# Optimization experiments

Hardware: AMD Instinct MI355X
Metric: run time of the kernel (lower is better)

Reference implementation:

```python
import jax, jax.numpy as jnp
import numpy as np

N = 50000          # neuron_count
NNZ = 1_600_000    # edges (avg degree 32)
B = 32             # batch
L = 3              # CONNECTOME_LAYER_NUMBER


def setup_inputs() -> dict:
    key = jax.random.key(0)
    k1, k2, k3, k4, k5 = jax.random.split(key, 5)
    x = jax.random.normal(k1, (B, N), dtype=jnp.float32)
    adj_vals = jax.random.uniform(k2, (NNZ,), dtype=jnp.float32)
    w_vals = jax.random.uniform(k3, (NNZ,), dtype=jnp.float32)
    bias = jnp.ones((N,), dtype=jnp.float32)
    row = jax.random.randint(k4, (NNZ,), 0, N, dtype=jnp.int32)
    col = jax.random.randint(k5, (NNZ,), 0, N, dtype=jnp.int32)
    return {"x": x, "adj_vals": adj_vals, "w_vals": w_vals, "bias": bias,
            "row": row, "col": col}


def _spmm(vals, row, col, dense, n):
    # (sparse NxN) @ dense [N, B] via gather + segment_sum scatter
    contrib = vals[:, None] * dense[col]          # [nnz, B]
    return jax.ops.segment_sum(contrib, row, num_segments=n)


def reference(x, adj_vals, w_vals, bias, row, col):
    # Original per layer: x = ((A @ W) @ x^T)^T + bias.
    # We use associativity: (A @ W) @ x^T == A @ (W @ x^T), avoiding the
    # explicit SpGEMM while computing the same linear map.
    n = bias.shape[0]
    xt = x.T                                      # [N, B]
    for _ in range(L):
        wx = _spmm(w_vals, row, col, xt, n)       # W @ x^T -> [N, B]
        xt = _spmm(adj_vals, row, col, wx, n)     # A @ (W @ x^T)
        xt = xt + bias[:, None]                   # broadcast bias over batch
    return xt.T                                   # [B, N]
```

## Files before the change

### kernel.cpp

```cpp
#include <hip/hip_runtime.h>


#define NN 50000
#define NNZ_E 1600000
#define NB (NN * 32)
#define CHUNK 3072
#define NBLK1 ((NNZ_E + CHUNK - 1) / CHUNK)
#define NBIN ((NN + 127) / 128)
#define CAP2 5120
#define BCAP1 6144
#define LENE (NBIN * BCAP1)
#define BCAP 6144
#define LENP (NBIN * BCAP)
#define TIN_BLKS 196

__device__ __forceinline__ int clampi(int v, int hi) {
    v = v < 0 ? 0 : v;
    return v > hi ? hi : v;
}

__device__ __forceinline__ unsigned short f2h(float v) {
    union { _Float16 h; unsigned short u; } cv;
    cv.h = (_Float16)v;
    return cv.u;
}

__device__ __forceinline__ float kv_val(unsigned kv) {
    union { unsigned short u; _Float16 h; } cv;
    cv.u = (unsigned short)(kv >> 16);
    return (float)cv.h;
}

__global__ __launch_bounds__(256) void pass1_kernel(
        const int* __restrict__ row, const int* __restrict__ col,
        const float* __restrict__ a, const float* __restrict__ w,
        int* __restrict__ cursor, uint2* __restrict__ e1,
        const float* __restrict__ x, _Float16* __restrict__ xt) {
    __shared__ unsigned sBuf[256 * 33 / 2 + 8];
    int blk = blockIdx.x, tid = threadIdx.x;

    if (blk >= NBLK1) {
        _Float16* tl = (_Float16*)sBuf;
        int n0 = (blk - NBLK1) * 256;
        int n = n0 + tid;
#pragma unroll 8
        for (int b = 0; b < 32; ++b) {
            float v = (n < NN) ? x[b * NN + n] : 0.0f;
            tl[tid * 33 + b] = (_Float16)v;
        }
        __syncthreads();
#pragma unroll
        for (int k = 0; k < 4; ++k) {
            int o = (tid + 256 * k) * 8;
            int nl = o >> 5;
            int b0 = o & 31;
            int nn = n0 + nl;
            if (nn < NN) {
                union { uint4 u4; _Float16 hh[8]; } pk;
#pragma unroll
                for (int j = 0; j < 8; ++j) pk.hh[j] = tl[nl * 33 + b0 + j];
                *(uint4*)&xt[nn * 32 + b0] = pk.u4;
            }
        }
        return;
    }

    int* h = (int*)sBuf;
    int base = blk * CHUNK;
    int n = NNZ_E - base; if (n > CHUNK) n = CHUNK;
    int nv = n >> 2;

    for (int j = tid; j < NBIN; j += 256) h[j] = 0;
    __syncthreads();

    int rr[12], cc[12];
    unsigned aw2[12];
    int ne = 0;
    const int4*   rv4 = (const int4*)row;
    const int4*   cv4 = (const int4*)col;
    const float4* av4 = (const float4*)a;
    const float4* wv4 = (const float4*)w;
    int b4 = base >> 2;
    for (int t4 = tid; t4 < nv; t4 += 256) {
        int4 r = rv4[b4 + t4];
        int4 c = cv4[b4 + t4];
        float4 af = av4[b4 + t4];
        float4 wf = wv4[b4 + t4];
        rr[ne] = r.x; cc[ne] = c.x; aw2[ne] = ((unsigned)f2h(af.x) << 16) | f2h(wf.x); ++ne;
        rr[ne] = r.y; cc[ne] = c.y; aw2[ne] = ((unsigned)f2h(af.y) << 16) | f2h(wf.y); ++ne;
        rr[ne] = r.z; cc[ne] = c.z; aw2[ne] = ((unsigned)f2h(af.z) << 16) | f2h(wf.z); ++ne;
        rr[ne] = r.w; cc[ne] = c.w; aw2[ne] = ((unsigned)f2h(af.w) << 16) | f2h(wf.w); ++ne;
    }
    for (int i = 0; i < ne; ++i)
        atomicAdd(&h[clampi(rr[i], NN - 1) >> 7], 1);
    __syncthreads();

    int j0 = tid * 2, j1 = tid * 2 + 1;
    if (j0 < NBIN) {
        int c0 = h[j0];
        int b0 = c0 ? atomicAdd(&cursor[j0], c0) : 0;
        h[j0] = j0 * BCAP1 + clampi(b0, BCAP1 - 1);
    }
    if (j1 < NBIN) {
        int c1 = h[j1];
        int b1 = c1 ? atomicAdd(&cursor[j1], c1) : 0;
        h[j1] = j1 * BCAP1 + clampi(b1, BCAP1 - 1);
    }
    __syncthreads();

    for (int i = 0; i < ne; ++i) {
        int r = clampi(rr[i], NN - 1);
        int c = clampi(cc[i], NN - 1);
        int bin = r >> 7;
        int d = atomicAdd(&h[bin], 1);
        d = clampi(d, LENE - 1);
        e1[d] = make_uint2(((unsigned)r << 16) | (unsigned)c, aw2[i]);
    }
}

__global__ __launch_bounds__(256) void pass2_kernel(
        const uint2* __restrict__ e1, const int* __restrict__ cursor,
        unsigned* __restrict__ kvA2, unsigned* __restrict__ kvW2,
        unsigned* __restrict__ row_desc) {
    __shared__ int rh[128];
    __shared__ int rs[128];
    __shared__ int cur[128];
    int bin = blockIdx.x, tid = threadIdx.x;
    int r0 = bin << 7;
    int rows = NN - r0; if (rows > 128) rows = 128;
    int ebase = bin * BCAP1;
    int size = clampi(cursor[bin], CAP2);
    int pbase = bin * BCAP;

    if (tid < 128) rh[tid] = 0;
    __syncthreads();
    for (int i = tid; i < size; i += 256)
        atomicAdd(&rh[(e1[ebase + i].x >> 16) & 127], 1);
    __syncthreads();
    int cnt  = (tid < 128) ? rh[tid] : 0;
    int plen = (cnt + 7) & ~7;
    if (tid < 128) rs[tid] = plen;
    __syncthreads();
    for (int off = 1; off < 128; off <<= 1) {
        int t = (tid >= off && tid < 128) ? rs[tid - off] : 0;
        __syncthreads();
        if (tid < 128) rs[tid] += t;
        __syncthreads();
    }
    int rofs = (tid < 128) ? clampi(rs[tid] - plen, BCAP - 8) : 0;
    if (tid < 128) cur[tid] = rofs;
    if (tid < rows)
        row_desc[r0 + tid] = (unsigned)(pbase + rofs) | ((unsigned)(plen >> 3) << 24);
    __syncthreads();
    for (int i = tid; i < size; i += 256) {
        uint2 e = e1[ebase + i];
        unsigned key = e.x;
        unsigned aw  = e.y;
        int rl = (key >> 16) & 127;
        int p = atomicAdd(&cur[rl], 1);
        p = clampi(p, BCAP - 1);
        unsigned c = key & 0xFFFFu;
        kvA2[pbase + p] = (aw & 0xFFFF0000u) | c;
        kvW2[pbase + p] = (aw << 16) | c;
    }
    __syncthreads();
    if (tid < rows) {
        int pl = (rh[tid] + 7) & ~7;
        for (int q = rh[tid]; q < pl; ++q) {
            int d = clampi(rofs + q, BCAP - 1);
            kvA2[pbase + d] = 0u;
            kvW2[pbase + d] = 0u;
        }
    }
}

template <int WITH_BIAS, int FINAL>
__global__ __launch_bounds__(256) void spmm_kernel(
        const uint2* __restrict__ kv2, const unsigned* __restrict__ row_desc,
        const unsigned* __restrict__ in32, unsigned* __restrict__ out32,
        const float* __restrict__ bias, float outScale, float biasScale,
        float* __restrict__ outf) {
    int t = blockIdx.x * 256 + threadIdx.x;
    int r = t >> 4;
    int l = t & 15;
    if (r >= NN) return;
    unsigned d = row_desc[r];
    int niter = (int)(d >> 24);
    int base2 = clampi((int)(d & 0xFFFFFFu), LENP - 8) >> 1;
    float accL = 0.0f, accH = 0.0f;
    uint2 k2[4];
    if (niter > 0) {
#pragma unroll
        for (int q = 0; q < 4; ++q) k2[q] = kv2[base2 + q];
    }
    for (int it = 0; it < niter; ++it) {
        unsigned k[8];
#pragma unroll
        for (int q = 0; q < 4; ++q) { k[2 * q] = k2[q].x; k[2 * q + 1] = k2[q].y; }
        unsigned gd[8];
#pragma unroll
        for (int j = 0; j < 8; ++j) gd[j] = in32[((k[j] & 0xFFFFu) << 4) + l];
        if (it + 1 < niter) {
            int nb2 = base2 + (it + 1) * 4;
#pragma unroll
            for (int q = 0; q < 4; ++q) k2[q] = kv2[nb2 + q];
        }
#pragma unroll
        for (int j = 0; j < 8; ++j) {
            float v = kv_val(k[j]);
            union { unsigned u; _Float16 h[2]; } cv;
            cv.u = gd[j];
            accL += v * (float)cv.h[0];
            accH += v * (float)cv.h[1];
        }
    }
    float rL = accL * outScale, rH = accH * outScale;
    if (WITH_BIAS) {
        float bb = bias[r] * biasScale;
        rL += bb; rH += bb;
    }
    if (FINAL) {
        outf[(2 * l) * NN + r]     = rL * 16777216.0f;
        outf[(2 * l + 1) * NN + r] = rH * 16777216.0f;
    } else {
        union { unsigned u; _Float16 h[2]; } o;
        o.h[0] = (_Float16)rL;
        o.h[1] = (_Float16)rH;
        out32[(r << 4) + l] = o.u;
    }
}

extern "C" void kernel_launch(void* const* d_in, const int* in_sizes, int n_in,
                              void* d_out, int out_size, void* d_ws, size_t ws_size,
                              hipStream_t stream) {
    const float* x        = (const float*)d_in[0];
    const float* adj_vals = (const float*)d_in[1];
    const float* w_vals   = (const float*)d_in[2];
    const float* bias     = (const float*)d_in[3];
    const int*   row      = (const int*)d_in[4];
    const int*   col      = (const int*)d_in[5];
    float* out = (float*)d_out;

    uint2*     e1        = (uint2*)d_ws;
    unsigned*  kvA2      = (unsigned*)(e1 + LENE);
    unsigned*  kvW2      = kvA2 + LENP;
    _Float16*  xt16      = (_Float16*)(kvW2 + LENP);
    _Float16*  tmp16     = xt16 + NB;
    int*       cursor    = (int*)(tmp16 + NB);
    unsigned*  row_desc  = (unsigned*)(cursor + NBIN + 8);

    const int BS = 256;
    const int grid_spmm = (NN * 16 + BS - 1) / BS;

    hipMemsetAsync(cursor, 0, NBIN * sizeof(int), stream);
    pass1_kernel<<<NBLK1 + TIN_BLKS, BS, 0, stream>>>(row, col, adj_vals, w_vals,
                                                      cursor, e1, x, xt16);
    pass2_kernel<<<NBIN, BS, 0, stream>>>(e1, cursor, kvA2, kvW2, row_desc);

    const uint2* kvA = (const uint2*)kvA2;
    const uint2* kvW = (const uint2*)kvW2;
    const unsigned* xt32  = (const unsigned*)xt16;
    unsigned*       xt32w = (unsigned*)xt16;
    const unsigned* tm32  = (const unsigned*)tmp16;
    unsigned*       tm32w = (unsigned*)tmp16;

    const float r256 = 1.0f / 256.0f;
    spmm_kernel<0, 0><<<grid_spmm, BS, 0, stream>>>(kvW, row_desc, xt32, tm32w,
                                                    nullptr, 1.0f, 0.0f, nullptr);
    spmm_kernel<1, 0><<<grid_spmm, BS, 0, stream>>>(kvA, row_desc, tm32, xt32w,
                                                    bias, r256, 1.0f / 256.0f, nullptr);
    spmm_kernel<0, 0><<<grid_spmm, BS, 0, stream>>>(kvW, row_desc, xt32, tm32w,
                                                    nullptr, 1.0f, 0.0f, nullptr);
    spmm_kernel<1, 0><<<grid_spmm, BS, 0, stream>>>(kvA, row_desc, tm32, xt32w,
                                                    bias, r256, 1.0f / 65536.0f, nullptr);
    spmm_kernel<0, 0><<<grid_spmm, BS, 0, stream>>>(kvW, row_desc, xt32, tm32w,
                                                    nullptr, 1.0f, 0.0f, nullptr);
    spmm_kernel<1, 1><<<grid_spmm, BS, 0, stream>>>(kvA, row_desc, tm32, xt32w,
                                                    bias, r256, 1.0f / 16777216.0f, out);
}
```

Baseline: 238.0 us.

## Bucket edges into 256-row windows with smaller chunks; pass2 filters per 128-row bin

Pass1 now buckets edges into 256-row windows instead of 128-row bins, which halves the shared histogram and the global cursor atomics per block. It also halves the chunk size to give more, lighter blocks, and moves the transpose blocks to the front of the grid. Pass2 blocks each read their whole window and filter out edges belonging to the neighbouring bin. That filtering doubles pass2's reads of the intermediate edge buffer in exchange for less contention and better balance in pass1.

```diff
diff --git a/kernel.cpp b/kernel.cpp
--- a/kernel.cpp
+++ b/kernel.cpp
@@ -4,12 +4,14 @@
 #define NN 50000
 #define NNZ_E 1600000
 #define NB (NN * 32)
-#define CHUNK 3072
+#define CHUNK 1536
 #define NBLK1 ((NNZ_E + CHUNK - 1) / CHUNK)
+#define NWIN ((NN + 255) / 256)
 #define NBIN ((NN + 127) / 128)
+#define CAP2W 10240
+#define BCAP1W 12288
+#define LENE (NWIN * BCAP1W)
 #define CAP2 5120
-#define BCAP1 6144
-#define LENE (NBIN * BCAP1)
 #define BCAP 6144
 #define LENP (NBIN * BCAP)
 #define TIN_BLKS 196
@@ -39,9 +41,9 @@
     __shared__ unsigned sBuf[256 * 33 / 2 + 8];
     int blk = blockIdx.x, tid = threadIdx.x;
 
-    if (blk >= NBLK1) {
+    if (blk < TIN_BLKS) {
         _Float16* tl = (_Float16*)sBuf;
-        int n0 = (blk - NBLK1) * 256;
+        int n0 = blk * 256;
         int n = n0 + tid;
 #pragma unroll 8
         for (int b = 0; b < 32; ++b) {
@@ -66,15 +68,15 @@
     }
 
     int* h = (int*)sBuf;
-    int base = blk * CHUNK;
+    int base = (blk - TIN_BLKS) * CHUNK;
     int n = NNZ_E - base; if (n > CHUNK) n = CHUNK;
     int nv = n >> 2;
 
-    for (int j = tid; j < NBIN; j += 256) h[j] = 0;
-    __syncthreads();
-
-    int rr[12], cc[12];
-    unsigned aw2[12];
+    for (int j = tid; j < NWIN; j += 256) h[j] = 0;
+    __syncthreads();
+
+    int rr[8], cc[8];
+    unsigned aw2[8];
     int ne = 0;
     const int4*   rv4 = (const int4*)row;
     const int4*   cv4 = (const int4*)col;
@@ -92,27 +94,21 @@
         rr[ne] = r.w; cc[ne] = c.w; aw2[ne] = ((unsigned)f2h(af.w) << 16) | f2h(wf.w); ++ne;
     }
     for (int i = 0; i < ne; ++i)
-        atomicAdd(&h[clampi(rr[i], NN - 1) >> 7], 1);
-    __syncthreads();
-
-    int j0 = tid * 2, j1 = tid * 2 + 1;
-    if (j0 < NBIN) {
-        int c0 = h[j0];
-        int b0 = c0 ? atomicAdd(&cursor[j0], c0) : 0;
-        h[j0] = j0 * BCAP1 + clampi(b0, BCAP1 - 1);
-    }
-    if (j1 < NBIN) {
-        int c1 = h[j1];
-        int b1 = c1 ? atomicAdd(&cursor[j1], c1) : 0;
-        h[j1] = j1 * BCAP1 + clampi(b1, BCAP1 - 1);
+        atomicAdd(&h[clampi(rr[i], NN - 1) >> 8], 1);
+    __syncthreads();
+
+    if (tid < NWIN) {
+        int c0 = h[tid];
+        int b0 = c0 ? atomicAdd(&cursor[tid], c0) : 0;
+        h[tid] = tid * BCAP1W + clampi(b0, BCAP1W - 1);
     }
     __syncthreads();
 
     for (int i = 0; i < ne; ++i) {
         int r = clampi(rr[i], NN - 1);
         int c = clampi(cc[i], NN - 1);
-        int bin = r >> 7;
-        int d = atomicAdd(&h[bin], 1);
+        int wb = r >> 8;
+        int d = atomicAdd(&h[wb], 1);
         d = clampi(d, LENE - 1);
         e1[d] = make_uint2(((unsigned)r << 16) | (unsigned)c, aw2[i]);
     }
@@ -128,16 +124,19 @@
     int bin = blockIdx.x, tid = threadIdx.x;
     int r0 = bin << 7;
     int rows = NN - r0; if (rows > 128) rows = 128;
-    int ebase = bin * BCAP1;
-    int size = clampi(cursor[bin], CAP2);
+    int win = bin >> 1;
+    int ebase = win * BCAP1W;
+    int size = clampi(cursor[win], CAP2W);
     int pbase = bin * BCAP;
 
     if (tid < 128) rh[tid] = 0;
     __syncthreads();
-    for (int i = tid; i < size; i += 256)
-        atomicAdd(&rh[(e1[ebase + i].x >> 16) & 127], 1);
-    __syncthreads();
-    int cnt  = (tid < 128) ? rh[tid] : 0;
+    for (int i = tid; i < size; i += 256) {
+        int rr = (int)(e1[ebase + i].x >> 16);
+        if ((rr >> 7) == bin) atomicAdd(&rh[rr & 127], 1);
+    }
+    __syncthreads();
+    int cnt  = (tid < 128) ? clampi(rh[tid], CAP2) : 0;
     int plen = (cnt + 7) & ~7;
     if (tid < 128) rs[tid] = plen;
     __syncthreads();
@@ -155,9 +154,10 @@
     for (int i = tid; i < size; i += 256) {
         uint2 e = e1[ebase + i];
         unsigned key = e.x;
-        unsigned aw  = e.y;
-        int rl = (key >> 16) & 127;
-        int p = atomicAdd(&cur[rl], 1);
+        int rr = (int)(key >> 16);
+        if ((rr >> 7) != bin) continue;
+        unsigned aw = e.y;
+        int p = atomicAdd(&cur[rr & 127], 1);
         p = clampi(p, BCAP - 1);
         unsigned c = key & 0xFFFFu;
         kvA2[pbase + p] = (aw & 0xFFFF0000u) | c;
@@ -165,8 +165,9 @@
     }
     __syncthreads();
     if (tid < rows) {
-        int pl = (rh[tid] + 7) & ~7;
-        for (int q = rh[tid]; q < pl; ++q) {
+        int cnt2 = clampi(rh[tid], CAP2);
+        int pl = (cnt2 + 7) & ~7;
+        for (int q = cnt2; q < pl; ++q) {
             int d = clampi(rofs + q, BCAP - 1);
             kvA2[pbase + d] = 0u;
             kvW2[pbase + d] = 0u;
@@ -247,13 +248,13 @@
     _Float16*  xt16      = (_Float16*)(kvW2 + LENP);
     _Float16*  tmp16     = xt16 + NB;
     int*       cursor    = (int*)(tmp16 + NB);
-    unsigned*  row_desc  = (unsigned*)(cursor + NBIN + 8);
+    unsigned*  row_desc  = (unsigned*)(cursor + NWIN + 8);
 
     const int BS = 256;
     const int grid_spmm = (NN * 16 + BS - 1) / BS;
 
-    hipMemsetAsync(cursor, 0, NBIN * sizeof(int), stream);
-    pass1_kernel<<<NBLK1 + TIN_BLKS, BS, 0, stream>>>(row, col, adj_vals, w_vals,
+    hipMemsetAsync(cursor, 0, NWIN * sizeof(int), stream);
+    pass1_kernel<<<TIN_BLKS + NBLK1, BS, 0, stream>>>(row, col, adj_vals, w_vals,
                                                       cursor, e1, x, xt16);
     pass2_kernel<<<NBIN, BS, 0, stream>>>(e1, cursor, kvA2, kvW2, row_desc);
 
```

Measured after the change: 237.7 us. About the same (-0.1%).
